# Performance work log

Measured on AMD Instinct MI355X. Metric: run time of the kernel, lower is better.

Reference implementation:

```python
import jax, jax.numpy as jnp
import numpy as np
import math

D_MODEL = 1024
H = 16
D_K = D_MODEL // H          # 64
D_HALF = D_MODEL // 2       # 512
DH = D_HALF // H            # 32 (half head dim for q/k)
B, S = 2, 1024
LAMBDA_INIT = 0.8 - 0.6 * math.exp(-0.3 * (1 - 1))  # layer_index=1 -> 0.2


def setup_inputs() -> dict:
    key = jax.random.key(0)
    ks = jax.random.split(key, 20)
    def lin(kk, fan_in, fan_out):
        lim = 1.0 / math.sqrt(fan_in)
        kw, kb = jax.random.split(kk)
        W = jax.random.uniform(kw, (fan_in, fan_out), jnp.float32, -lim, lim)
        b = jax.random.uniform(kb, (fan_out,), jnp.float32, -lim, lim)
        return W, b
    Wq1, bq1 = lin(ks[0], D_MODEL, D_HALF)
    Wq2, bq2 = lin(ks[1], D_MODEL, D_HALF)
    Wk1, bk1 = lin(ks[2], D_MODEL, D_HALF)
    Wk2, bk2 = lin(ks[3], D_MODEL, D_HALF)
    Wv, bv = lin(ks[4], D_MODEL, D_MODEL)
    Wo, bo = lin(ks[5], D_MODEL, D_MODEL)
    q = jax.random.normal(ks[6], (B, S, D_MODEL), jnp.float32)
    k = jax.random.normal(ks[7], (B, S, D_MODEL), jnp.float32)
    v = jax.random.normal(ks[8], (B, S, D_MODEL), jnp.float32)
    # causal 0/1 mask, already 4-D [B,1,S,S]
    mask = jnp.broadcast_to(jnp.tril(jnp.ones((S, S), jnp.int32)), (B, 1, S, S))
    # small random lambda scalars (torch inits to 0 -> degenerate gradients)
    lq1 = jax.random.normal(ks[9], (1,), jnp.float32) * 0.1
    lk1 = jax.random.normal(ks[10], (1,), jnp.float32) * 0.1
    lq2 = jax.random.normal(ks[11], (1,), jnp.float32) * 0.1
    lk2 = jax.random.normal(ks[12], (1,), jnp.float32) * 0.1
    return dict(q=q, k=k, v=v, mask=mask,
                Wq1=Wq1, bq1=bq1, Wq2=Wq2, bq2=bq2,
                Wk1=Wk1, bk1=bk1, Wk2=Wk2, bk2=bk2,
                Wv=Wv, bv=bv, Wo=Wo, bo=bo,
                lq1=lq1, lk1=lk1, lq2=lq2, lk2=lk2)


def reference(q, k, v, mask, Wq1, bq1, Wq2, bq2, Wk1, bk1, Wk2, bk2,
              Wv, bv, Wo, bo, lq1, lk1, lq2, lk2):
    b, sq, _ = q.shape
    sk = k.shape[1]
    # projections, reshaped to [B, S, H, head_dim]
    q1 = (q @ Wq1 + bq1).reshape(b, sq, H, DH)
    q2 = (q @ Wq2 + bq2).reshape(b, sq, H, DH)
    k1 = (k @ Wk1 + bk1).reshape(b, sk, H, DH)
    k2 = (k @ Wk2 + bk2).reshape(b, sk, H, DH)
    vv = (v @ Wv + bv).reshape(b, sk, H, D_K)
    lam = jnp.exp(lq1 * lk1) - jnp.exp(lq2 * lk2) + LAMBDA_INIT  # shape (1,)
    scale = 1.0 / math.sqrt(D_K)
    s1 = jnp.einsum('bqhd,bkhd->bhqk', q1, k1) * scale
    s2 = jnp.einsum('bqhd,bkhd->bhqk', q2, k2) * scale
    neg = jnp.float32(-1e9)
    keep = mask != 0  # [B,1,Sq,Sk], broadcasts over heads
    s1 = jnp.where(keep, s1, neg)
    s2 = jnp.where(keep, s2, neg)
    a1 = jax.nn.softmax(s1, axis=-1)
    a2 = jax.nn.softmax(s2, axis=-1)
    diff = a1 - lam[0] * a2  # dropout p=0.0 -> identity
    out = jnp.einsum('bhqk,bkhd->bqhd', diff, vv).reshape(b, sq, D_MODEL)
    return out @ Wo + bo
```

## Files before the change

### kernel.cpp

```cpp
#include <hip/hip_runtime.h>
#include <hip/hip_bf16.h>
#include <cstdint>
#include <cstddef>

typedef __attribute__((ext_vector_type(8))) short short8;
typedef __attribute__((ext_vector_type(4))) float floatx4;

#define B_ 2
#define S_ 1024
#define H_ 16
#define DM_ 1024
#define DHALF_ 512
#define DH_ 32
#define DK_ 64
#define LAMBDA_INIT_ 0.2f
#define SCALE_ 0.125f
#define M_INIT_ -1.0e4f
#define MASK_NEG_ -1.0e9f

static __device__ __forceinline__ unsigned short f2bf(float f) {
  uint32_t u = __float_as_uint(f);
  uint32_t r = (u + 0x7fffu + ((u >> 16) & 1u)) >> 16;
  return (unsigned short)r;
}

static __device__ __forceinline__ uint32_t pkbf(float a, float b) {
  __hip_bfloat162 h = __float22bfloat162_rn(make_float2(a, b));
  return *reinterpret_cast<uint32_t*>(&h);
}

static __device__ __forceinline__ void gload16(const void* g, void* l) {
  __builtin_amdgcn_global_load_lds(
      (const __attribute__((address_space(1))) uint32_t*)g,
      (__attribute__((address_space(3))) uint32_t*)l, 16, 0, 0);
}

__global__ __launch_bounds__(256) void prep_kernel(
    const float* __restrict__ q, const float* __restrict__ k, const float* __restrict__ v,
    const float* __restrict__ Wq1, const float* __restrict__ Wq2,
    const float* __restrict__ Wk1, const float* __restrict__ Wk2,
    const float* __restrict__ Wv, const float* __restrict__ Wo,
    const float* __restrict__ bq1, const float* __restrict__ bq2,
    const float* __restrict__ bk1, const float* __restrict__ bk2,
    unsigned short* __restrict__ WqT, unsigned short* __restrict__ WkT,
    unsigned short* __restrict__ WvT, unsigned short* __restrict__ WoT,
    unsigned short* __restrict__ qbf, unsigned short* __restrict__ kbf,
    unsigned short* __restrict__ vbf,
    float* __restrict__ biasQ, float* __restrict__ biasK)
{
  __shared__ float tile[64][65];
  const int bid = blockIdx.x;
  const int tid = threadIdx.x;
  if (bid < 1024) {
    const float* W; unsigned short* WT; int ncols, n_off, local;
    if (bid < 128)      { W = Wq1; WT = WqT; ncols = 512;  n_off = 0;   local = bid; }
    else if (bid < 256) { W = Wq2; WT = WqT; ncols = 512;  n_off = 512; local = bid - 128; }
    else if (bid < 384) { W = Wk1; WT = WkT; ncols = 512;  n_off = 0;   local = bid - 256; }
    else if (bid < 512) { W = Wk2; WT = WkT; ncols = 512;  n_off = 512; local = bid - 384; }
    else if (bid < 768) { W = Wv;  WT = WvT; ncols = 1024; n_off = 0;   local = bid - 512; }
    else                { W = Wo;  WT = WoT; ncols = 1024; n_off = 0;   local = bid - 768; }
    const int ntiles = ncols >> 6;
    const int n0 = (local % ntiles) * 64;
    const int k0 = (local / ntiles) * 64;
#pragma unroll
    for (int i = 0; i < 4; ++i) {
      int idx = tid + 256 * i;
      int r = idx >> 4, c4 = idx & 15;
      float4 val = *reinterpret_cast<const float4*>(W + (size_t)(k0 + r) * ncols + n0 + c4 * 4);
      tile[r][c4 * 4 + 0] = val.x; tile[r][c4 * 4 + 1] = val.y;
      tile[r][c4 * 4 + 2] = val.z; tile[r][c4 * 4 + 3] = val.w;
    }
    __syncthreads();
#pragma unroll
    for (int i = 0; i < 2; ++i) {
      int G = tid + 256 * i;
      int n = G >> 3, g = G & 7;
      short8 o;
#pragma unroll
      for (int j = 0; j < 8; ++j) o[j] = (short)f2bf(tile[g * 8 + j][n]);
      *reinterpret_cast<short8*>(WT + (size_t)(n_off + n0 + n) * 1024 + k0 + g * 8) = o;
    }
  } else if (bid < 4096) {
    int local = bid - 1024;
    int t = local >> 10;
    int i = local & 1023;
    const float* src = (t == 0) ? q : ((t == 1) ? k : v);
    unsigned short* dst = (t == 0) ? qbf : ((t == 1) ? kbf : vbf);
    const int base = i * 2048 + tid * 8;
    float4 a = *reinterpret_cast<const float4*>(src + base);
    float4 b2 = *reinterpret_cast<const float4*>(src + base + 4);
    short8 o;
    o[0] = (short)f2bf(a.x);  o[1] = (short)f2bf(a.y);
    o[2] = (short)f2bf(a.z);  o[3] = (short)f2bf(a.w);
    o[4] = (short)f2bf(b2.x); o[5] = (short)f2bf(b2.y);
    o[6] = (short)f2bf(b2.z); o[7] = (short)f2bf(b2.w);
    *reinterpret_cast<short8*>(dst + base) = o;
  } else {
#pragma unroll
    for (int j = 0; j < 4; ++j) {
      int i = j * 256 + tid;
      biasQ[i] = (i < 512) ? bq1[i] : bq2[i - 512];
      biasK[i] = (i < 512) ? bk1[i] : bk2[i - 512];
    }
  }
}

template<int ROWS>
static __device__ __forceinline__ void stage_rows(
    const unsigned short* __restrict__ G, int row0, int kk0,
    unsigned short* L, int tid)
{
#pragma unroll
  for (int i = 0; i < ROWS / 32; ++i) {
    const int o = i * 4096 + tid * 16;
    const int r = o >> 7;
    const int c = ((o >> 4) & 7) ^ (r & 7);
    gload16(G + (size_t)(row0 + r) * 1024 + kk0 + c * 8, L + (o >> 1));
  }
}

template<int BM, int BN>
static __device__ __forceinline__ void gemm_mainloop(
    const unsigned short* __restrict__ A, const unsigned short* __restrict__ BT,
    int m0, int n0,
    unsigned short* As0, unsigned short* As1,
    unsigned short* Bs0, unsigned short* Bs1,
    floatx4 (&acc)[BM / 32][BN / 32])
{
  constexpr int MT = BM / 32, NT = BN / 32;
  const int tid = threadIdx.x;
  const int lane = tid & 63;
  const int l15 = lane & 15, hi = lane >> 4;
  const int wid = tid >> 6;
  const int wr = wid >> 1, wc = wid & 1;

  stage_rows<BM>(A, m0, 0, As0, tid);
  stage_rows<BN>(BT, n0, 0, Bs0, tid);
  __syncthreads();

  for (int ks = 0; ks < 16; ++ks) {
    unsigned short* Ac = (ks & 1) ? As1 : As0;
    unsigned short* Bc = (ks & 1) ? Bs1 : Bs0;
    unsigned short* An = (ks & 1) ? As0 : As1;
    unsigned short* Bn = (ks & 1) ? Bs0 : Bs1;
    if (ks < 15) {
      stage_rows<BM>(A, m0, (ks + 1) * 64, An, tid);
      stage_rows<BN>(BT, n0, (ks + 1) * 64, Bn, tid);
    }
#pragma unroll
    for (int kk = 0; kk < 2; ++kk) {
      short8 af[MT], bf[NT];
#pragma unroll
      for (int mt = 0; mt < MT; ++mt) {
        const int r = wr * (BM / 2) + mt * 16 + l15;
        af[mt] = *reinterpret_cast<const short8*>(Ac + r * 64 + (((kk * 4 + hi) ^ (r & 7)) << 3));
      }
#pragma unroll
      for (int nt = 0; nt < NT; ++nt) {
        const int r = wc * (BN / 2) + nt * 16 + l15;
        bf[nt] = *reinterpret_cast<const short8*>(Bc + r * 64 + (((kk * 4 + hi) ^ (r & 7)) << 3));
      }
#pragma unroll
      for (int mt = 0; mt < MT; ++mt)
#pragma unroll
        for (int nt = 0; nt < NT; ++nt)
          acc[mt][nt] = __builtin_amdgcn_mfma_f32_16x16x32_bf16(af[mt], bf[nt], acc[mt][nt], 0, 0, 0);
    }
    __syncthreads();
  }
}

__global__ __launch_bounds__(256) void proj_gemm_kernel(
    const unsigned short* __restrict__ qbf, const unsigned short* __restrict__ kbf,
    const unsigned short* __restrict__ vbf,
    const unsigned short* __restrict__ WqT, const unsigned short* __restrict__ WkT,
    const unsigned short* __restrict__ WvT,
    const float* __restrict__ biasQ, const float* __restrict__ biasK,
    const float* __restrict__ bv,
    unsigned short* __restrict__ q12b, unsigned short* __restrict__ k12b,
    unsigned short* __restrict__ vvT)
{
  __shared__ unsigned short As[2][128 * 64];
  __shared__ unsigned short Bs[2][64 * 64];
  const int z = blockIdx.z;
  const unsigned short* A = (z == 0) ? qbf : ((z == 1) ? kbf : vbf);
  const unsigned short* BT = (z == 0) ? WqT : ((z == 1) ? WkT : WvT);
  const float* bias = (z == 0) ? biasQ : ((z == 1) ? biasK : bv);
  const int n0 = blockIdx.x * 64;
  const int m0 = blockIdx.y * 128;
  const int lane = threadIdx.x & 63, wid = threadIdx.x >> 6;
  const int l15 = lane & 15, hi = lane >> 4;
  const int wr = wid >> 1, wc = wid & 1;

  floatx4 acc[4][2];
#pragma unroll
  for (int a = 0; a < 4; ++a)
#pragma unroll
    for (int c = 0; c < 2; ++c) acc[a][c] = (floatx4){0.f, 0.f, 0.f, 0.f};

  gemm_mainloop<128, 64>(A, BT, m0, n0, As[0], As[1], Bs[0], Bs[1], acc);

#pragma unroll
  for (int nt = 0; nt < 2; ++nt) {
    const int n = n0 + wc * 32 + nt * 16 + l15;
    const float bn = bias[n];
#pragma unroll
    for (int mt = 0; mt < 4; ++mt) {
      const int mrow = m0 + wr * 64 + mt * 16 + 4 * hi;
      if (z < 2) {
        unsigned short* dst = (z == 0 ? q12b : k12b);
#pragma unroll
        for (int r = 0; r < 4; ++r)
          dst[(size_t)(mrow + r) * 1024 + n] = f2bf(acc[mt][nt][r] + bn);
      } else {
        const int bb = mrow >> 10, ss = mrow & 1023;
        const int hh = n >> 6, dd = n & 63;
        float v0 = acc[mt][nt][0] + bn, v1 = acc[mt][nt][1] + bn;
        float v2 = acc[mt][nt][2] + bn, v3 = acc[mt][nt][3] + bn;
        uint2 pk;
        pk.x = pkbf(v0, v1);
        pk.y = pkbf(v2, v3);
        *reinterpret_cast<uint2*>(vvT + ((size_t)(bb * 16 + hh) * 64 + dd) * 1024 + ss) = pk;
      }
    }
  }
}

__global__ __launch_bounds__(256) void out_gemm_kernel(
    const unsigned short* __restrict__ Ab, const unsigned short* __restrict__ BT,
    const float* __restrict__ bias, float* __restrict__ out)
{
  __shared__ unsigned short As[2][64 * 64];
  __shared__ unsigned short Bs[2][64 * 64];
  const int n0 = blockIdx.x * 64;
  const int m0 = blockIdx.y * 64;
  const int lane = threadIdx.x & 63, wid = threadIdx.x >> 6;
  const int l15 = lane & 15, hi = lane >> 4;
  const int wr = wid >> 1, wc = wid & 1;

  floatx4 acc[2][2];
#pragma unroll
  for (int a = 0; a < 2; ++a)
#pragma unroll
    for (int c = 0; c < 2; ++c) acc[a][c] = (floatx4){0.f, 0.f, 0.f, 0.f};

  gemm_mainloop<64, 64>(Ab, BT, m0, n0, As[0], As[1], Bs[0], Bs[1], acc);

#pragma unroll
  for (int nt = 0; nt < 2; ++nt) {
    const int n = n0 + wc * 32 + nt * 16 + l15;
    const float bn = bias[n];
#pragma unroll
    for (int mt = 0; mt < 2; ++mt) {
      const int mrow = m0 + wr * 32 + mt * 16 + 4 * hi;
#pragma unroll
      for (int r = 0; r < 4; ++r)
        out[(size_t)(mrow + r) * 1024 + n] = acc[mt][nt][r] + bn;
    }
  }
}

#define STAGE_KV(kbase_, bi_)                                                  \
  {                                                                            \
    const size_t krow0_ = (size_t)(b * S_ + (kbase_));                         \
    _Pragma("unroll")                                                          \
    for (int i_ = 0; i_ < 4; ++i_) {                                           \
      const int o_ = i_ * 4096 + tid * 16;              \
      const int kr_ = o_ >> 7;                         \
      const int kc_ = ((o_ >> 4) & 7) ^ (kr_ & 7);                             \
      const unsigned short* ks_ = (kc_ < 4)                                    \
          ? (k12b + (krow0_ + kr_) * DM_ + h * DH_ + kc_ * 8)                  \
          : (k12b + (krow0_ + kr_) * DM_ + DHALF_ + h * DH_ + (kc_ - 4) * 8);  \
      gload16(ks_, &Kt[bi_][0] + (o_ >> 1));                                   \
      const int vr_ = o_ >> 8;                          \
      const int vc_ = ((o_ >> 4) & 15) ^ (vr_ & 15);                           \
      gload16(vvT + (vrow0 + vr_) * (size_t)S_ + (kbase_) + vc_ * 8,           \
              &Vt[bi_][0] + (o_ >> 1));                                        \
    }                                                                          \
  }

__global__ __launch_bounds__(256) void diff_attn_kernel(
    const unsigned short* __restrict__ q12b, const unsigned short* __restrict__ k12b,
    const unsigned short* __restrict__ vvT, unsigned short* __restrict__ attn,
    const float* __restrict__ lq1, const float* __restrict__ lk1,
    const float* __restrict__ lq2, const float* __restrict__ lk2)
{
  __shared__ unsigned short Kt[2][128 * 64];
  __shared__ unsigned short Vt[2][64 * 128];
  __shared__ unsigned short Pl[4][2][16 * 64];

  const int tid = threadIdx.x;
  const int lane = tid & 63, wid = tid >> 6;
  const int l15 = lane & 15, hi = lane >> 4;

  const int idx = blockIdx.x;
  const int hf = idx >> 8;
  const int pk = idx & 255;
  const int h = pk & 15;
  const int b = (pk >> 4) & 1;
  const int j = pk >> 5;
  const int qblk = hf ? (15 - j) : j;

  const int qbase = qblk * 64 + wid * 16;
  const float lam = __expf(lq1[0] * lk1[0]) - __expf(lq2[0] * lk2[0]) + LAMBDA_INIT_;
  const size_t vrow0 = (size_t)(b * H_ + h) * DK_;

  const size_t qrow = (size_t)(b * S_ + qbase + l15) * DM_;
  const short8 q1f = *reinterpret_cast<const short8*>(q12b + qrow + h * DH_ + hi * 8);
  const short8 q2f = *reinterpret_cast<const short8*>(q12b + qrow + DHALF_ + h * DH_ + hi * 8);

  floatx4 acc1[4], acc2[4];
#pragma unroll
  for (int dt = 0; dt < 4; ++dt) {
    acc1[dt] = (floatx4){0.f, 0.f, 0.f, 0.f};
    acc2[dt] = (floatx4){0.f, 0.f, 0.f, 0.f};
  }
  float m1 = M_INIT_, m2 = M_INIT_, l1 = 0.f, l2 = 0.f;

  unsigned short* P1 = &Pl[wid][0][0];
  unsigned short* P2 = &Pl[wid][1][0];

  const int ntiles = (qblk >> 1) + 1;
  STAGE_KV(0, 0);
  __syncthreads();

  for (int kb = 0; kb < ntiles; ++kb) {
    const int cur = kb & 1;
    const int kbase = kb * 128;
    if (kb + 1 < ntiles) STAGE_KV(kbase + 128, cur ^ 1);

    floatx4 s1[8], s2[8];
    const floatx4 zz = (floatx4){0.f, 0.f, 0.f, 0.f};
    __builtin_amdgcn_s_setprio(1);
#pragma unroll
    for (int t = 0; t < 8; ++t) {
      const int r = 16 * t + l15;
      short8 k1f = *reinterpret_cast<const short8*>(&Kt[cur][0] + r * 64 + ((hi ^ (r & 7)) << 3));
      short8 k2f = *reinterpret_cast<const short8*>(&Kt[cur][0] + r * 64 + (((hi + 4) ^ (r & 7)) << 3));
      s1[t] = __builtin_amdgcn_mfma_f32_16x16x32_bf16(k1f, q1f, zz, 0, 0, 0);
      s2[t] = __builtin_amdgcn_mfma_f32_16x16x32_bf16(k2f, q2f, zz, 0, 0, 0);
    }
    __builtin_amdgcn_s_setprio(0);

    if (kb == ntiles - 1) {
      const int qg = qbase + l15;
#pragma unroll
      for (int t = 0; t < 8; ++t) {
#pragma unroll
        for (int e = 0; e < 4; ++e) {
          const int kg = kbase + 16 * t + 4 * hi + e;
          if (kg > qg) { s1[t][e] = MASK_NEG_; s2[t][e] = MASK_NEG_; }
        }
      }
    }

    float tm1, tm2;
    {
      float x1 = fmaxf(fmaxf(s1[0][0], s1[0][1]), fmaxf(s1[0][2], s1[0][3]));
      float x2 = fmaxf(fmaxf(s2[0][0], s2[0][1]), fmaxf(s2[0][2], s2[0][3]));
#pragma unroll
      for (int t = 1; t < 8; ++t) {
        x1 = fmaxf(x1, fmaxf(fmaxf(s1[t][0], s1[t][1]), fmaxf(s1[t][2], s1[t][3])));
        x2 = fmaxf(x2, fmaxf(fmaxf(s2[t][0], s2[t][1]), fmaxf(s2[t][2], s2[t][3])));
      }
      tm1 = x1; tm2 = x2;
    }
    tm1 = fmaxf(tm1, __shfl_xor(tm1, 16));
    tm1 = fmaxf(tm1, __shfl_xor(tm1, 32));
    tm2 = fmaxf(tm2, __shfl_xor(tm2, 16));
    tm2 = fmaxf(tm2, __shfl_xor(tm2, 32));

    const float nm1 = fmaxf(m1, tm1);
    const float nm2 = fmaxf(m2, tm2);
    const float sc1 = __expf((m1 - nm1) * SCALE_);
    const float sc2 = __expf((m2 - nm2) * SCALE_);
    m1 = nm1; m2 = nm2;
#pragma unroll
    for (int dt = 0; dt < 4; ++dt) { acc1[dt] *= sc1; acc2[dt] *= sc2; }

    float rs1 = 0.f, rs2 = 0.f;
#pragma unroll
    for (int half = 0; half < 2; ++half) {
#pragma unroll
      for (int tt = 0; tt < 4; ++tt) {
        const int t = half * 4 + tt;
        float p10 = __expf((s1[t][0] - m1) * SCALE_);
        float p11 = __expf((s1[t][1] - m1) * SCALE_);
        float p12 = __expf((s1[t][2] - m1) * SCALE_);
        float p13 = __expf((s1[t][3] - m1) * SCALE_);
        rs1 += (p10 + p11) + (p12 + p13);
        float p20 = __expf((s2[t][0] - m2) * SCALE_);
        float p21 = __expf((s2[t][1] - m2) * SCALE_);
        float p22 = __expf((s2[t][2] - m2) * SCALE_);
        float p23 = __expf((s2[t][3] - m2) * SCALE_);
        rs2 += (p20 + p21) + (p22 + p23);
        const int idx2 = l15 * 64 + (((2 * tt + (hi >> 1)) ^ (l15 & 7)) << 3) + ((hi & 1) << 2);
        uint2 w1; w1.x = pkbf(p10, p11); w1.y = pkbf(p12, p13);
        *reinterpret_cast<uint2*>(P1 + idx2) = w1;
        uint2 w2; w2.x = pkbf(p20, p21); w2.y = pkbf(p22, p23);
        *reinterpret_cast<uint2*>(P2 + idx2) = w2;
      }
      __builtin_amdgcn_s_setprio(1);
#pragma unroll
      for (int kc = 0; kc < 2; ++kc) {
        short8 p1f = *reinterpret_cast<const short8*>(P1 + l15 * 64 + (((hi + 4 * kc) ^ (l15 & 7)) << 3));
        short8 p2f = *reinterpret_cast<const short8*>(P2 + l15 * 64 + (((hi + 4 * kc) ^ (l15 & 7)) << 3));
#pragma unroll
        for (int dt = 0; dt < 4; ++dt) {
          const int d = dt * 16 + l15;
          short8 vf = *reinterpret_cast<const short8*>(
              &Vt[cur][0] + d * 128 + (((hi + 4 * (2 * half + kc)) ^ (d & 15)) << 3));
          acc1[dt] = __builtin_amdgcn_mfma_f32_16x16x32_bf16(vf, p1f, acc1[dt], 0, 0, 0);
          acc2[dt] = __builtin_amdgcn_mfma_f32_16x16x32_bf16(vf, p2f, acc2[dt], 0, 0, 0);
        }
      }
      __builtin_amdgcn_s_setprio(0);
    }
    rs1 += __shfl_xor(rs1, 16);
    rs1 += __shfl_xor(rs1, 32);
    rs2 += __shfl_xor(rs2, 16);
    rs2 += __shfl_xor(rs2, 32);
    l1 = l1 * sc1 + rs1;
    l2 = l2 * sc2 + rs2;

    __syncthreads();
  }

  const float inv1 = 1.0f / l1;
  const float inv2 = lam / l2;
  const int qg = qbase + l15;
  unsigned short* op = attn + (size_t)(b * S_ + qg) * DM_ + h * DK_;
#pragma unroll
  for (int dt = 0; dt < 4; ++dt) {
    float o0 = acc1[dt][0] * inv1 - acc2[dt][0] * inv2;
    float o1 = acc1[dt][1] * inv1 - acc2[dt][1] * inv2;
    float o2 = acc1[dt][2] * inv1 - acc2[dt][2] * inv2;
    float o3 = acc1[dt][3] * inv1 - acc2[dt][3] * inv2;
    uint2 pkv;
    pkv.x = pkbf(o0, o1);
    pkv.y = pkbf(o2, o3);
    *reinterpret_cast<uint2*>(op + dt * 16 + 4 * hi) = pkv;
  }
}

extern "C" void kernel_launch(void* const* d_in, const int* in_sizes, int n_in,
                              void* d_out, int out_size, void* d_ws, size_t ws_size,
                              hipStream_t stream)
{
  const float* q   = (const float*)d_in[0];
  const float* k   = (const float*)d_in[1];
  const float* v   = (const float*)d_in[2];
  const float* Wq1 = (const float*)d_in[4];
  const float* bq1 = (const float*)d_in[5];
  const float* Wq2 = (const float*)d_in[6];
  const float* bq2 = (const float*)d_in[7];
  const float* Wk1 = (const float*)d_in[8];
  const float* bk1 = (const float*)d_in[9];
  const float* Wk2 = (const float*)d_in[10];
  const float* bk2 = (const float*)d_in[11];
  const float* Wv  = (const float*)d_in[12];
  const float* bv  = (const float*)d_in[13];
  const float* Wo  = (const float*)d_in[14];
  const float* bo  = (const float*)d_in[15];
  const float* lq1 = (const float*)d_in[16];
  const float* lk1 = (const float*)d_in[17];
  const float* lq2 = (const float*)d_in[18];
  const float* lk2 = (const float*)d_in[19];
  float* out = (float*)d_out;

  uint8_t* w = (uint8_t*)d_ws;
  unsigned short* WqT  = (unsigned short*)w; w += (size_t)2 * 1024 * 1024;
  unsigned short* WkT  = (unsigned short*)w; w += (size_t)2 * 1024 * 1024;
  unsigned short* WvT  = (unsigned short*)w; w += (size_t)2 * 1024 * 1024;
  unsigned short* WoT  = (unsigned short*)w; w += (size_t)2 * 1024 * 1024;
  unsigned short* qbf  = (unsigned short*)w; w += (size_t)4 * 1024 * 1024;
  unsigned short* kbf  = (unsigned short*)w; w += (size_t)4 * 1024 * 1024;
  unsigned short* vbf  = (unsigned short*)w; w += (size_t)4 * 1024 * 1024;
  unsigned short* q12b = (unsigned short*)w; w += (size_t)4 * 1024 * 1024;
  unsigned short* k12b = (unsigned short*)w; w += (size_t)4 * 1024 * 1024;
  unsigned short* vvT  = (unsigned short*)w; w += (size_t)4 * 1024 * 1024;
  float* biasQ = (float*)w; w += 4096;
  float* biasK = (float*)w; w += 4096;
  unsigned short* attnb = qbf;

  dim3 blk(256);
  hipLaunchKernelGGL(prep_kernel, dim3(4097), blk, 0, stream,
                     q, k, v, Wq1, Wq2, Wk1, Wk2, Wv, Wo,
                     bq1, bq2, bk1, bk2,
                     WqT, WkT, WvT, WoT, qbf, kbf, vbf, biasQ, biasK);

  hipLaunchKernelGGL(proj_gemm_kernel, dim3(16, 16, 3), blk, 0, stream,
                     qbf, kbf, vbf, WqT, WkT, WvT, biasQ, biasK, bv,
                     q12b, k12b, vvT);

  hipLaunchKernelGGL(diff_attn_kernel, dim3(512), blk, 0, stream,
                     q12b, k12b, vvT, attnb, lq1, lk1, lq2, lk2);

  hipLaunchKernelGGL(out_gemm_kernel, dim3(16, 32), blk, 0, stream,
                     attnb, WoT, bo, out);
}
```

Baseline: 78.27 us.

## Split the two softmax streams across separate waves in diff attention

The attention block grows from 256 to 512 threads, and each pair of waves now splits the two differential softmax streams (q1/k1 and q2/k2) for the same 16 query rows. Each wave keeps one accumulator set and one running max/sum, which roughly halves per-wave register pressure and serial work and doubles wave-level parallelism per block. At the end the second-stream wave writes its scaled output to shared memory, reusing the K buffer, and the first-stream wave combines and stores the result. This adds a block-wide sync and duplicates the V fragment loads and P·V MFMAs across the two waves.

Result: faster. 71.46 us (-8.7%).

```diff
diff --git a/kernel.cpp b/kernel.cpp
--- a/kernel.cpp
+++ b/kernel.cpp
@@ -264,8 +264,8 @@
   {                                                                            \
     const size_t krow0_ = (size_t)(b * S_ + (kbase_));                         \
     _Pragma("unroll")                                                          \
-    for (int i_ = 0; i_ < 4; ++i_) {                                           \
-      const int o_ = i_ * 4096 + tid * 16;              \
+    for (int i_ = 0; i_ < 2; ++i_) {                                           \
+      const int o_ = i_ * 8192 + tid * 16;              \
       const int kr_ = o_ >> 7;                         \
       const int kc_ = ((o_ >> 4) & 7) ^ (kr_ & 7);                             \
       const unsigned short* ks_ = (kc_ < 4)                                    \
@@ -279,7 +279,7 @@
     }                                                                          \
   }
 
-__global__ __launch_bounds__(256) void diff_attn_kernel(
+__global__ __launch_bounds__(512) void diff_attn_kernel(
     const unsigned short* __restrict__ q12b, const unsigned short* __restrict__ k12b,
     const unsigned short* __restrict__ vvT, unsigned short* __restrict__ attn,
     const float* __restrict__ lq1, const float* __restrict__ lk1,
@@ -287,10 +287,12 @@
 {
   __shared__ unsigned short Kt[2][128 * 64];
   __shared__ unsigned short Vt[2][64 * 128];
-  __shared__ unsigned short Pl[4][2][16 * 64];
+  __shared__ unsigned short Pl[8][16 * 64];
 
   const int tid = threadIdx.x;
   const int lane = tid & 63, wid = tid >> 6;
+  const int st = wid & 1;
+  const int qw = wid >> 1;
   const int l15 = lane & 15, hi = lane >> 4;
 
   const int idx = blockIdx.x;
@@ -301,24 +303,20 @@
   const int j = pk >> 5;
   const int qblk = hf ? (15 - j) : j;
 
-  const int qbase = qblk * 64 + wid * 16;
+  const int qbase = qblk * 64 + qw * 16;
   const float lam = __expf(lq1[0] * lk1[0]) - __expf(lq2[0] * lk2[0]) + LAMBDA_INIT_;
   const size_t vrow0 = (size_t)(b * H_ + h) * DK_;
 
   const size_t qrow = (size_t)(b * S_ + qbase + l15) * DM_;
-  const short8 q1f = *reinterpret_cast<const short8*>(q12b + qrow + h * DH_ + hi * 8);
-  const short8 q2f = *reinterpret_cast<const short8*>(q12b + qrow + DHALF_ + h * DH_ + hi * 8);
-
-  floatx4 acc1[4], acc2[4];
-#pragma unroll
-  for (int dt = 0; dt < 4; ++dt) {
-    acc1[dt] = (floatx4){0.f, 0.f, 0.f, 0.f};
-    acc2[dt] = (floatx4){0.f, 0.f, 0.f, 0.f};
-  }
-  float m1 = M_INIT_, m2 = M_INIT_, l1 = 0.f, l2 = 0.f;
-
-  unsigned short* P1 = &Pl[wid][0][0];
-  unsigned short* P2 = &Pl[wid][1][0];
+  const short8 qf = *reinterpret_cast<const short8*>(
+      q12b + qrow + st * DHALF_ + h * DH_ + hi * 8);
+
+  floatx4 acc[4];
+#pragma unroll
+  for (int dt = 0; dt < 4; ++dt) acc[dt] = (floatx4){0.f, 0.f, 0.f, 0.f};
+  float m = M_INIT_, l = 0.f;
+
+  unsigned short* P = &Pl[wid][0];
 
   const int ntiles = (qblk >> 1) + 1;
   STAGE_KV(0, 0);
@@ -329,16 +327,15 @@
     const int kbase = kb * 128;
     if (kb + 1 < ntiles) STAGE_KV(kbase + 128, cur ^ 1);
 
-    floatx4 s1[8], s2[8];
+    floatx4 s[8];
     const floatx4 zz = (floatx4){0.f, 0.f, 0.f, 0.f};
     __builtin_amdgcn_s_setprio(1);
 #pragma unroll
     for (int t = 0; t < 8; ++t) {
       const int r = 16 * t + l15;
-      short8 k1f = *reinterpret_cast<const short8*>(&Kt[cur][0] + r * 64 + ((hi ^ (r & 7)) << 3));
-      short8 k2f = *reinterpret_cast<const short8*>(&Kt[cur][0] + r * 64 + (((hi + 4) ^ (r & 7)) << 3));
-      s1[t] = __builtin_amdgcn_mfma_f32_16x16x32_bf16(k1f, q1f, zz, 0, 0, 0);
-      s2[t] = __builtin_amdgcn_mfma_f32_16x16x32_bf16(k2f, q2f, zz, 0, 0, 0);
+      short8 kf = *reinterpret_cast<const short8*>(
+          &Kt[cur][0] + r * 64 + (((hi + 4 * st) ^ (r & 7)) << 3));
+      s[t] = __builtin_amdgcn_mfma_f32_16x16x32_bf16(kf, qf, zz, 0, 0, 0);
     }
     __builtin_amdgcn_s_setprio(0);
 
@@ -349,97 +346,93 @@
 #pragma unroll
         for (int e = 0; e < 4; ++e) {
           const int kg = kbase + 16 * t + 4 * hi + e;
-          if (kg > qg) { s1[t][e] = MASK_NEG_; s2[t][e] = MASK_NEG_; }
+          if (kg > qg) s[t][e] = MASK_NEG_;
         }
       }
     }
 
-    float tm1, tm2;
+    float tm;
     {
-      float x1 = fmaxf(fmaxf(s1[0][0], s1[0][1]), fmaxf(s1[0][2], s1[0][3]));
-      float x2 = fmaxf(fmaxf(s2[0][0], s2[0][1]), fmaxf(s2[0][2], s2[0][3]));
-#pragma unroll
-      for (int t = 1; t < 8; ++t) {
-        x1 = fmaxf(x1, fmaxf(fmaxf(s1[t][0], s1[t][1]), fmaxf(s1[t][2], s1[t][3])));
-        x2 = fmaxf(x2, fmaxf(fmaxf(s2[t][0], s2[t][1]), fmaxf(s2[t][2], s2[t][3])));
-      }
-      tm1 = x1; tm2 = x2;
-    }
-    tm1 = fmaxf(tm1, __shfl_xor(tm1, 16));
-    tm1 = fmaxf(tm1, __shfl_xor(tm1, 32));
-    tm2 = fmaxf(tm2, __shfl_xor(tm2, 16));
-    tm2 = fmaxf(tm2, __shfl_xor(tm2, 32));
-
-    const float nm1 = fmaxf(m1, tm1);
-    const float nm2 = fmaxf(m2, tm2);
-    const float sc1 = __expf((m1 - nm1) * SCALE_);
-    const float sc2 = __expf((m2 - nm2) * SCALE_);
-    m1 = nm1; m2 = nm2;
-#pragma unroll
-    for (int dt = 0; dt < 4; ++dt) { acc1[dt] *= sc1; acc2[dt] *= sc2; }
-
-    float rs1 = 0.f, rs2 = 0.f;
+      float x = fmaxf(fmaxf(s[0][0], s[0][1]), fmaxf(s[0][2], s[0][3]));
+#pragma unroll
+      for (int t = 1; t < 8; ++t)
+        x = fmaxf(x, fmaxf(fmaxf(s[t][0], s[t][1]), fmaxf(s[t][2], s[t][3])));
+      tm = x;
+    }
+    tm = fmaxf(tm, __shfl_xor(tm, 16));
+    tm = fmaxf(tm, __shfl_xor(tm, 32));
+
+    const float nm = fmaxf(m, tm);
+    const float sc = __expf((m - nm) * SCALE_);
+    m = nm;
+#pragma unroll
+    for (int dt = 0; dt < 4; ++dt) acc[dt] *= sc;
+
+    float rs = 0.f;
 #pragma unroll
     for (int half = 0; half < 2; ++half) {
 #pragma unroll
       for (int tt = 0; tt < 4; ++tt) {
         const int t = half * 4 + tt;
-        float p10 = __expf((s1[t][0] - m1) * SCALE_);
-        float p11 = __expf((s1[t][1] - m1) * SCALE_);
-        float p12 = __expf((s1[t][2] - m1) * SCALE_);
-        float p13 = __expf((s1[t][3] - m1) * SCALE_);
-        rs1 += (p10 + p11) + (p12 + p13);
-        float p20 = __expf((s2[t][0] - m2) * SCALE_);
-        float p21 = __expf((s2[t][1] - m2) * SCALE_);
-        float p22 = __expf((s2[t][2] - m2) * SCALE_);
-        float p23 = __expf((s2[t][3] - m2) * SCALE_);
-        rs2 += (p20 + p21) + (p22 + p23);
+        float p0 = __expf((s[t][0] - m) * SCALE_);
+        float p1 = __expf((s[t][1] - m) * SCALE_);
+        float p2 = __expf((s[t][2] - m) * SCALE_);
+        float p3 = __expf((s[t][3] - m) * SCALE_);
+        rs += (p0 + p1) + (p2 + p3);
         const int idx2 = l15 * 64 + (((2 * tt + (hi >> 1)) ^ (l15 & 7)) << 3) + ((hi & 1) << 2);
-        uint2 w1; w1.x = pkbf(p10, p11); w1.y = pkbf(p12, p13);
-        *reinterpret_cast<uint2*>(P1 + idx2) = w1;
-        uint2 w2; w2.x = pkbf(p20, p21); w2.y = pkbf(p22, p23);
-        *reinterpret_cast<uint2*>(P2 + idx2) = w2;
+        uint2 w1; w1.x = pkbf(p0, p1); w1.y = pkbf(p2, p3);
+        *reinterpret_cast<uint2*>(P + idx2) = w1;
       }
       __builtin_amdgcn_s_setprio(1);
 #pragma unroll
       for (int kc = 0; kc < 2; ++kc) {
-        short8 p1f = *reinterpret_cast<const short8*>(P1 + l15 * 64 + (((hi + 4 * kc) ^ (l15 & 7)) << 3));
-        short8 p2f = *reinterpret_cast<const short8*>(P2 + l15 * 64 + (((hi + 4 * kc) ^ (l15 & 7)) << 3));
+        short8 pf = *reinterpret_cast<const short8*>(
+            P + l15 * 64 + (((hi + 4 * kc) ^ (l15 & 7)) << 3));
 #pragma unroll
         for (int dt = 0; dt < 4; ++dt) {
           const int d = dt * 16 + l15;
           short8 vf = *reinterpret_cast<const short8*>(
               &Vt[cur][0] + d * 128 + (((hi + 4 * (2 * half + kc)) ^ (d & 15)) << 3));
-          acc1[dt] = __builtin_amdgcn_mfma_f32_16x16x32_bf16(vf, p1f, acc1[dt], 0, 0, 0);
-          acc2[dt] = __builtin_amdgcn_mfma_f32_16x16x32_bf16(vf, p2f, acc2[dt], 0, 0, 0);
+          acc[dt] = __builtin_amdgcn_mfma_f32_16x16x32_bf16(vf, pf, acc[dt], 0, 0, 0);
         }
       }
       __builtin_amdgcn_s_setprio(0);
     }
-    rs1 += __shfl_xor(rs1, 16);
-    rs1 += __shfl_xor(rs1, 32);
-    rs2 += __shfl_xor(rs2, 16);
-    rs2 += __shfl_xor(rs2, 32);
-    l1 = l1 * sc1 + rs1;
-    l2 = l2 * sc2 + rs2;
+    rs += __shfl_xor(rs, 16);
+    rs += __shfl_xor(rs, 32);
+    l = l * sc + rs;
 
     __syncthreads();
   }
 
-  const float inv1 = 1.0f / l1;
-  const float inv2 = lam / l2;
-  const int qg = qbase + l15;
-  unsigned short* op = attn + (size_t)(b * S_ + qg) * DM_ + h * DK_;
-#pragma unroll
-  for (int dt = 0; dt < 4; ++dt) {
-    float o0 = acc1[dt][0] * inv1 - acc2[dt][0] * inv2;
-    float o1 = acc1[dt][1] * inv1 - acc2[dt][1] * inv2;
-    float o2 = acc1[dt][2] * inv1 - acc2[dt][2] * inv2;
-    float o3 = acc1[dt][3] * inv1 - acc2[dt][3] * inv2;
-    uint2 pkv;
-    pkv.x = pkbf(o0, o1);
-    pkv.y = pkbf(o2, o3);
-    *reinterpret_cast<uint2*>(op + dt * 16 + 4 * hi) = pkv;
+  float* Os = reinterpret_cast<float*>(&Kt[0][0]);
+  if (st == 1) {
+    const float inv2 = lam / l;
+    float* dstp = Os + qw * (16 * 68) + l15 * 68;
+#pragma unroll
+    for (int dt = 0; dt < 4; ++dt) {
+#pragma unroll
+      for (int e = 0; e < 4; ++e)
+        dstp[dt * 16 + 4 * hi + e] = acc[dt][e] * inv2;
+    }
+  }
+  __syncthreads();
+  if (st == 0) {
+    const float inv1 = 1.0f / l;
+    const float* srcp = Os + qw * (16 * 68) + l15 * 68;
+    const int qg = qbase + l15;
+    unsigned short* op = attn + (size_t)(b * S_ + qg) * DM_ + h * DK_;
+#pragma unroll
+    for (int dt = 0; dt < 4; ++dt) {
+      float o0 = acc[dt][0] * inv1 - srcp[dt * 16 + 4 * hi + 0];
+      float o1 = acc[dt][1] * inv1 - srcp[dt * 16 + 4 * hi + 1];
+      float o2 = acc[dt][2] * inv1 - srcp[dt * 16 + 4 * hi + 2];
+      float o3 = acc[dt][3] * inv1 - srcp[dt * 16 + 4 * hi + 3];
+      uint2 pkv;
+      pkv.x = pkbf(o0, o1);
+      pkv.y = pkbf(o2, o3);
+      *reinterpret_cast<uint2*>(op + dt * 16 + 4 * hi) = pkv;
+    }
   }
 }
 
@@ -493,7 +486,7 @@
                      qbf, kbf, vbf, WqT, WkT, WvT, biasQ, biasK, bv,
                      q12b, k12b, vvT);
 
-  hipLaunchKernelGGL(diff_attn_kernel, dim3(512), blk, 0, stream,
+  hipLaunchKernelGGL(diff_attn_kernel, dim3(512), dim3(512), 0, stream,
                      q12b, k12b, vvT, attnb, lq1, lk1, lq2, lk2);
 
   hipLaunchKernelGGL(out_gemm_kernel, dim3(16, 32), blk, 0, stream,
```
